# Optimization experiments

Hardware: AMD Instinct MI355X
Metric: run time of the kernel (lower is better)

Reference implementation:

```python
import jax, jax.numpy as jnp
import numpy as np

N = 100000
E = 3200000
H = 128
C = 40


def setup_inputs() -> dict:
    key = jax.random.key(0)
    ks = jax.random.split(key, 7)
    x = jax.random.normal(ks[0], (N, H), dtype=jnp.float32)
    edge_src = jax.random.randint(ks[1], (E,), 0, N, dtype=jnp.int32)
    edge_dst = jnp.sort(jax.random.randint(ks[2], (E,), 0, N, dtype=jnp.int32))
    edge_w = jax.random.uniform(ks[3], (E,), dtype=jnp.float32)
    s = 1.0 / np.sqrt(H)
    W0 = jax.random.normal(ks[4], (H, H), dtype=jnp.float32) * s
    W1 = jax.random.normal(ks[5], (H, H), dtype=jnp.float32) * s
    W2 = jax.random.normal(ks[6], (H, C), dtype=jnp.float32) * s
    return {"x": x, "edge_src": edge_src, "edge_dst": edge_dst,
            "edge_w": edge_w, "W0": W0, "W1": W1, "W2": W2}


def _spmm(h, edge_src, edge_dst, edge_w):
    # out[i] = sum_{e: dst_e == i} w_e * h[src_e]   (sparse adj @ h)
    msgs = h[edge_src] * edge_w[:, None]          # [E, d]
    return jax.ops.segment_sum(msgs, edge_dst, num_segments=N)


def reference(x, edge_src, edge_dst, edge_w, W0, W1, W2):
    # layer 1: tanh(Linear(spmm(adj, x)))  (dropout is identity in eval mode)
    h = jnp.tanh(_spmm(x, edge_src, edge_dst, edge_w) @ W0)
    # layer 2
    h = jnp.tanh(_spmm(h, edge_src, edge_dst, edge_w) @ W1)
    # output layer (GraphConvSparse default activation is tanh here too)
    out = jnp.tanh(_spmm(h, edge_src, edge_dst, edge_w) @ W2)
    return out
```

## Files before the change

### kernel.cpp

```cpp
#include <hip/hip_runtime.h>
#include <hip/hip_fp16.h>

#define NN 100000
#define NPAD 100096
#define EE 3200000
#define HH 128
#define CC 40

typedef _Float16 f16x8 __attribute__((ext_vector_type(8)));
typedef float f32x4 __attribute__((ext_vector_type(4)));

__global__ void build_rp(const int* __restrict__ dst, int* __restrict__ rp) {
    int i = blockIdx.x * blockDim.x + threadIdx.x;
    if (i > NN) return;
    int lo = 0, hi = EE;
    while (lo < hi) {
        int mid = (lo + hi) >> 1;
        if (dst[mid] < i) lo = mid + 1; else hi = mid;
    }
    rp[i] = lo;
}

__global__ __launch_bounds__(256) void f32_to_f16(const float* __restrict__ in,
                                                  __half* __restrict__ out, int n) {
    int base = (blockIdx.x * 256 + threadIdx.x) * 8;
    if (base >= n) return;
    float4 a = *(const float4*)(in + base);
    float4 b = *(const float4*)(in + base + 4);
    __half2 h[4];
    h[0] = __floats2half2_rn(a.x, a.y);
    h[1] = __floats2half2_rn(a.z, a.w);
    h[2] = __floats2half2_rn(b.x, b.y);
    h[3] = __floats2half2_rn(b.z, b.w);
    *(float4*)(out + base) = *(float4*)h;
}

__global__ __launch_bounds__(256) void prep_weights(const float* __restrict__ W0,
                                                    const float* __restrict__ W1,
                                                    const float* __restrict__ W2,
                                                    __half* __restrict__ W0t,
                                                    __half* __restrict__ W1t,
                                                    __half* __restrict__ W2t) {
    int i = blockIdx.x * 256 + threadIdx.x;
    if (i < HH * HH) {
        int c = i >> 7, k = i & 127;
        W0t[i] = __float2half_rn(W0[k * HH + c]);
        W1t[i] = __float2half_rn(W1[k * HH + c]);
    }
    if (i < 48 * HH) {
        int c = i >> 7, k = i & 127;
        W2t[i] = __float2half_rn(c < CC ? W2[k * CC + c] : 0.f);
    }
}

__global__ __launch_bounds__(256) void spmm_h16(const __half* __restrict__ h,
                                                const int* __restrict__ src,
                                                const float* __restrict__ w,
                                                const int* __restrict__ rp,
                                                __half* __restrict__ out) {
    int node = blockIdx.x * 4 + (threadIdx.x >> 6);
    int t = threadIdx.x & 63;
    if (node >= NN) return;
    int e0 = __builtin_amdgcn_readfirstlane(rp[node]);
    int e1 = __builtin_amdgcn_readfirstlane(rp[node + 1]);
    const __half2* __restrict__ h2 = (const __half2*)h;
    float accx = 0.f, accy = 0.f;
    int e = e0;
    for (; e + 8 <= e1; e += 8) {
        int s[8]; float wv[8]; __half2 r[8];
#pragma unroll
        for (int j = 0; j < 8; ++j) { s[j] = src[e + j]; wv[j] = w[e + j]; }
#pragma unroll
        for (int j = 0; j < 8; ++j) r[j] = h2[(size_t)s[j] * 64 + t];
#pragma unroll
        for (int j = 0; j < 8; ++j) {
            float2 f = __half22float2(r[j]);
            accx = fmaf(wv[j], f.x, accx);
            accy = fmaf(wv[j], f.y, accy);
        }
    }
    for (; e < e1; ++e) {
        int s = src[e]; float ww = w[e];
        float2 f = __half22float2(h2[(size_t)s * 64 + t]);
        accx = fmaf(ww, f.x, accx); accy = fmaf(ww, f.y, accy);
    }
    ((__half2*)out)[(size_t)node * 64 + t] = __floats2half2_rn(accx, accy);
}

__global__ __launch_bounds__(256) void spmm40_tanh(const __half* __restrict__ g,
                                                   const int* __restrict__ src,
                                                   const float* __restrict__ w,
                                                   const int* __restrict__ rp,
                                                   float* __restrict__ out) {
    int node = blockIdx.x * 4 + (threadIdx.x >> 6);
    int t = threadIdx.x & 63;
    if (node >= NN) return;
    int e0 = __builtin_amdgcn_readfirstlane(rp[node]);
    int e1 = __builtin_amdgcn_readfirstlane(rp[node + 1]);
    const __half2* __restrict__ g2 = (const __half2*)g;
    int tt = t < 20 ? t : 0;
    float accx = 0.f, accy = 0.f;
    int e = e0;
    for (; e + 8 <= e1; e += 8) {
        int s[8]; float wv[8]; __half2 r[8];
#pragma unroll
        for (int j = 0; j < 8; ++j) { s[j] = src[e + j]; wv[j] = w[e + j]; }
#pragma unroll
        for (int j = 0; j < 8; ++j) r[j] = g2[(size_t)s[j] * 20 + tt];
#pragma unroll
        for (int j = 0; j < 8; ++j) {
            float2 f = __half22float2(r[j]);
            accx = fmaf(wv[j], f.x, accx);
            accy = fmaf(wv[j], f.y, accy);
        }
    }
    for (; e < e1; ++e) {
        int s = src[e]; float ww = w[e];
        float2 f = __half22float2(g2[(size_t)s * 20 + tt]);
        accx = fmaf(ww, f.x, accx); accy = fmaf(ww, f.y, accy);
    }
    if (t < 20)
        *(float2*)(out + (size_t)node * CC + 2 * t) = make_float2(tanhf(accx), tanhf(accy));
}

__global__ __launch_bounds__(256) void gemm_mfma_tanh(const __half* __restrict__ A,
                                                      const __half* __restrict__ Wt,
                                                      __half* __restrict__ out) {
    int wave = threadIdx.x >> 6, l = threadIdx.x & 63;
    int r0 = blockIdx.x * 64 + wave * 16;
    int lr = l & 15, lg = l >> 4;
    const _Float16* Af = (const _Float16*)A;
    const _Float16* Wf = (const _Float16*)Wt;
    int arow = r0 + lr;
    f16x8 a[4];
#pragma unroll
    for (int kb = 0; kb < 4; ++kb)
        a[kb] = *(const f16x8*)(Af + (size_t)arow * HH + kb * 32 + lg * 8);
#pragma unroll
    for (int ct = 0; ct < 8; ++ct) {
        f32x4 acc = {0.f, 0.f, 0.f, 0.f};
#pragma unroll
        for (int kb = 0; kb < 4; ++kb) {
            f16x8 b = *(const f16x8*)(Wf + (size_t)(ct * 16 + lr) * HH + kb * 32 + lg * 8);
            acc = __builtin_amdgcn_mfma_f32_16x16x32_f16(a[kb], b, acc, 0, 0, 0);
        }
#pragma unroll
        for (int r = 0; r < 4; ++r) {
            int row = r0 + lg * 4 + r;
            if (row < NN)
                out[(size_t)row * HH + ct * 16 + lr] = __float2half_rn(tanhf(acc[r]));
        }
    }
}

__global__ __launch_bounds__(256) void gemm40_mfma(const __half* __restrict__ A,
                                                   const __half* __restrict__ Wt,
                                                   __half* __restrict__ out) {
    int wave = threadIdx.x >> 6, l = threadIdx.x & 63;
    int r0 = blockIdx.x * 64 + wave * 16;
    int lr = l & 15, lg = l >> 4;
    const _Float16* Af = (const _Float16*)A;
    const _Float16* Wf = (const _Float16*)Wt;
    int arow = r0 + lr;
    f16x8 a[4];
#pragma unroll
    for (int kb = 0; kb < 4; ++kb)
        a[kb] = *(const f16x8*)(Af + (size_t)arow * HH + kb * 32 + lg * 8);
#pragma unroll
    for (int ct = 0; ct < 3; ++ct) {
        f32x4 acc = {0.f, 0.f, 0.f, 0.f};
#pragma unroll
        for (int kb = 0; kb < 4; ++kb) {
            f16x8 b = *(const f16x8*)(Wf + (size_t)(ct * 16 + lr) * HH + kb * 32 + lg * 8);
            acc = __builtin_amdgcn_mfma_f32_16x16x32_f16(a[kb], b, acc, 0, 0, 0);
        }
        int col = ct * 16 + lr;
#pragma unroll
        for (int r = 0; r < 4; ++r) {
            int row = r0 + lg * 4 + r;
            if (row < NN && col < CC)
                out[(size_t)row * CC + col] = __float2half_rn(acc[r]);
        }
    }
}

extern "C" void kernel_launch(void* const* d_in, const int* in_sizes, int n_in,
                              void* d_out, int out_size, void* d_ws, size_t ws_size,
                              hipStream_t stream) {
    const float* x    = (const float*)d_in[0];
    const int*   esrc = (const int*)d_in[1];
    const int*   edst = (const int*)d_in[2];
    const float* ew   = (const float*)d_in[3];
    const float* W0   = (const float*)d_in[4];
    const float* W1   = (const float*)d_in[5];
    const float* W2   = (const float*)d_in[6];
    float* out = (float*)d_out;

    char* ws = (char*)d_ws;
    size_t off = 0;
    int* rp = (int*)(ws + off);          off += (((size_t)(NN + 1) * 4) + 511) & ~(size_t)511;
    __half* xh = (__half*)(ws + off);    off += (size_t)NPAD * HH * sizeof(__half);
    __half* sA = (__half*)(ws + off);    off += (size_t)NPAD * HH * sizeof(__half);
    __half* hb = (__half*)(ws + off);    off += (size_t)NPAD * HH * sizeof(__half);
    __half* gb = (__half*)(ws + off);    off += (size_t)NPAD * CC * sizeof(__half);
    __half* W0t = (__half*)(ws + off);   off += (size_t)HH * HH * sizeof(__half);
    __half* W1t = (__half*)(ws + off);   off += (size_t)HH * HH * sizeof(__half);
    __half* W2t = (__half*)(ws + off);   off += (size_t)48 * HH * sizeof(__half);

    build_rp<<<(NN + 256) / 256, 256, 0, stream>>>(edst, rp);
    f32_to_f16<<<(NN * HH) / (256 * 8), 256, 0, stream>>>(x, xh, NN * HH);
    prep_weights<<<64, 256, 0, stream>>>(W0, W1, W2, W0t, W1t, W2t);

    int gemm_grid = NPAD / 64;
    spmm_h16<<<NN / 4, 256, 0, stream>>>(xh, esrc, ew, rp, sA);
    gemm_mfma_tanh<<<gemm_grid, 256, 0, stream>>>(sA, W0t, hb);
    spmm_h16<<<NN / 4, 256, 0, stream>>>(hb, esrc, ew, rp, sA);
    gemm_mfma_tanh<<<gemm_grid, 256, 0, stream>>>(sA, W1t, hb);
    gemm40_mfma<<<gemm_grid, 256, 0, stream>>>(hb, W2t, gb);
    spmm40_tanh<<<NN / 4, 256, 0, stream>>>(gb, esrc, ew, rp, out);
}
```

Measured before the change: 498.8 us.

## Interleave edge src/weight and split SpMM edges across lane groups with wide loads

Adds a prep kernel that packs edge source indices and weights into interleaved int2 pairs. The SpMM kernels now have each wave split into lane groups that process different edges in parallel, with 16-byte f16x8 row loads, and then reduce the groups with cross-lane shuffles. The 40-column intermediate is padded to 64 columns so rows align for vector loads. This aims to raise memory-level parallelism and cut the number of per-edge index loads in the gather, at the cost of an extra edge-packing pass over 3.2M edges and shuffle reductions.

After: 514.6 us. 3.2% more time.

```diff
diff --git a/kernel.cpp b/kernel.cpp
--- a/kernel.cpp
+++ b/kernel.cpp
@@ -35,6 +35,19 @@
     *(float4*)(out + base) = *(float4*)h;
 }
 
+__global__ __launch_bounds__(256) void prep_edges(const int* __restrict__ src,
+                                                  const float* __restrict__ w,
+                                                  int4* __restrict__ ew) {
+    int i = blockIdx.x * 256 + threadIdx.x;
+    if (i >= EE / 4) return;
+    int4 s = ((const int4*)src)[i];
+    float4 f = ((const float4*)w)[i];
+    int4 a, b;
+    a.x = s.x; a.y = __float_as_int(f.x); a.z = s.y; a.w = __float_as_int(f.y);
+    b.x = s.z; b.y = __float_as_int(f.z); b.z = s.w; b.w = __float_as_int(f.w);
+    ew[2 * i] = a; ew[2 * i + 1] = b;
+}
+
 __global__ __launch_bounds__(256) void prep_weights(const float* __restrict__ W0,
                                                     const float* __restrict__ W1,
                                                     const float* __restrict__ W2,
@@ -47,80 +60,135 @@
         W0t[i] = __float2half_rn(W0[k * HH + c]);
         W1t[i] = __float2half_rn(W1[k * HH + c]);
     }
-    if (i < 48 * HH) {
+    if (i < 64 * HH) {
         int c = i >> 7, k = i & 127;
         W2t[i] = __float2half_rn(c < CC ? W2[k * CC + c] : 0.f);
     }
 }
 
 __global__ __launch_bounds__(256) void spmm_h16(const __half* __restrict__ h,
-                                                const int* __restrict__ src,
-                                                const float* __restrict__ w,
+                                                const int2* __restrict__ ew,
                                                 const int* __restrict__ rp,
                                                 __half* __restrict__ out) {
     int node = blockIdx.x * 4 + (threadIdx.x >> 6);
-    int t = threadIdx.x & 63;
+    int l = threadIdx.x & 63;
     if (node >= NN) return;
     int e0 = __builtin_amdgcn_readfirstlane(rp[node]);
     int e1 = __builtin_amdgcn_readfirstlane(rp[node + 1]);
-    const __half2* __restrict__ h2 = (const __half2*)h;
-    float accx = 0.f, accy = 0.f;
+    int g = l >> 4, r = l & 15;
+    const f16x8* __restrict__ hrow = (const f16x8*)h;
+    float acc[8] = {};
     int e = e0;
-    for (; e + 8 <= e1; e += 8) {
-        int s[8]; float wv[8]; __half2 r[8];
-#pragma unroll
-        for (int j = 0; j < 8; ++j) { s[j] = src[e + j]; wv[j] = w[e + j]; }
-#pragma unroll
-        for (int j = 0; j < 8; ++j) r[j] = h2[(size_t)s[j] * 64 + t];
-#pragma unroll
-        for (int j = 0; j < 8; ++j) {
-            float2 f = __half22float2(r[j]);
-            accx = fmaf(wv[j], f.x, accx);
-            accy = fmaf(wv[j], f.y, accy);
-        }
-    }
-    for (; e < e1; ++e) {
-        int s = src[e]; float ww = w[e];
-        float2 f = __half22float2(h2[(size_t)s * 64 + t]);
-        accx = fmaf(ww, f.x, accx); accy = fmaf(ww, f.y, accy);
-    }
-    ((__half2*)out)[(size_t)node * 64 + t] = __floats2half2_rn(accx, accy);
-}
-
-__global__ __launch_bounds__(256) void spmm40_tanh(const __half* __restrict__ g,
-                                                   const int* __restrict__ src,
-                                                   const float* __restrict__ w,
+    if ((e & 1) && e < e1) {
+        int2 pr = ew[e];
+        float wk = (g == 0) ? __int_as_float(pr.y) : 0.f;
+        f16x8 v = hrow[(size_t)pr.x * 16 + r];
+#pragma unroll
+        for (int j = 0; j < 8; ++j) acc[j] = fmaf(wk, (float)v[j], acc[j]);
+        ++e;
+    }
+    int efull = e + ((e1 - e) & ~15);
+    for (; e < efull; e += 16) {
+        const int4* pp = (const int4*)(ew + e + 4 * g);
+        int4 pa = pp[0];
+        int4 pb = pp[1];
+        f16x8 v0 = hrow[(size_t)pa.x * 16 + r];
+        f16x8 v1 = hrow[(size_t)pa.z * 16 + r];
+        f16x8 v2 = hrow[(size_t)pb.x * 16 + r];
+        f16x8 v3 = hrow[(size_t)pb.z * 16 + r];
+        float w0 = __int_as_float(pa.y), w1 = __int_as_float(pa.w);
+        float w2 = __int_as_float(pb.y), w3 = __int_as_float(pb.w);
+#pragma unroll
+        for (int j = 0; j < 8; ++j) acc[j] = fmaf(w0, (float)v0[j], acc[j]);
+#pragma unroll
+        for (int j = 0; j < 8; ++j) acc[j] = fmaf(w1, (float)v1[j], acc[j]);
+#pragma unroll
+        for (int j = 0; j < 8; ++j) acc[j] = fmaf(w2, (float)v2[j], acc[j]);
+#pragma unroll
+        for (int j = 0; j < 8; ++j) acc[j] = fmaf(w3, (float)v3[j], acc[j]);
+    }
+    if (e < e1) {
+#pragma unroll
+        for (int k = 0; k < 4; ++k) {
+            int idx = e + 4 * g + k;
+            bool val = idx < e1;
+            int2 pr = ew[val ? idx : e0];
+            float wk = val ? __int_as_float(pr.y) : 0.f;
+            f16x8 v = hrow[(size_t)pr.x * 16 + r];
+#pragma unroll
+            for (int j = 0; j < 8; ++j) acc[j] = fmaf(wk, (float)v[j], acc[j]);
+        }
+    }
+#pragma unroll
+    for (int j = 0; j < 8; ++j) {
+        acc[j] += __shfl_xor(acc[j], 16);
+        acc[j] += __shfl_xor(acc[j], 32);
+    }
+    if (l < 16) {
+        __half2 hv[4];
+#pragma unroll
+        for (int j = 0; j < 4; ++j) hv[j] = __floats2half2_rn(acc[2 * j], acc[2 * j + 1]);
+        *(float4*)(out + (size_t)node * HH + r * 8) = *(float4*)hv;
+    }
+}
+
+__global__ __launch_bounds__(256) void spmm40_tanh(const __half* __restrict__ gpad,
+                                                   const int2* __restrict__ ew,
                                                    const int* __restrict__ rp,
                                                    float* __restrict__ out) {
     int node = blockIdx.x * 4 + (threadIdx.x >> 6);
-    int t = threadIdx.x & 63;
+    int l = threadIdx.x & 63;
     if (node >= NN) return;
     int e0 = __builtin_amdgcn_readfirstlane(rp[node]);
     int e1 = __builtin_amdgcn_readfirstlane(rp[node + 1]);
-    const __half2* __restrict__ g2 = (const __half2*)g;
-    int tt = t < 20 ? t : 0;
-    float accx = 0.f, accy = 0.f;
+    int g = l >> 3, r = l & 7;
+    const f16x8* __restrict__ grow = (const f16x8*)gpad;
+    float acc[8] = {};
     int e = e0;
-    for (; e + 8 <= e1; e += 8) {
-        int s[8]; float wv[8]; __half2 r[8];
-#pragma unroll
-        for (int j = 0; j < 8; ++j) { s[j] = src[e + j]; wv[j] = w[e + j]; }
-#pragma unroll
-        for (int j = 0; j < 8; ++j) r[j] = g2[(size_t)s[j] * 20 + tt];
-#pragma unroll
-        for (int j = 0; j < 8; ++j) {
-            float2 f = __half22float2(r[j]);
-            accx = fmaf(wv[j], f.x, accx);
-            accy = fmaf(wv[j], f.y, accy);
-        }
-    }
-    for (; e < e1; ++e) {
-        int s = src[e]; float ww = w[e];
-        float2 f = __half22float2(g2[(size_t)s * 20 + tt]);
-        accx = fmaf(ww, f.x, accx); accy = fmaf(ww, f.y, accy);
-    }
-    if (t < 20)
-        *(float2*)(out + (size_t)node * CC + 2 * t) = make_float2(tanhf(accx), tanhf(accy));
+    if ((e & 1) && e < e1) {
+        int2 pr = ew[e];
+        float wk = (g == 0) ? __int_as_float(pr.y) : 0.f;
+        f16x8 v = grow[(size_t)pr.x * 8 + r];
+#pragma unroll
+        for (int j = 0; j < 8; ++j) acc[j] = fmaf(wk, (float)v[j], acc[j]);
+        ++e;
+    }
+    int efull = e + ((e1 - e) & ~15);
+    for (; e < efull; e += 16) {
+        int4 pa = *(const int4*)(ew + e + 2 * g);
+        f16x8 v0 = grow[(size_t)pa.x * 8 + r];
+        f16x8 v1 = grow[(size_t)pa.z * 8 + r];
+        float w0 = __int_as_float(pa.y), w1 = __int_as_float(pa.w);
+#pragma unroll
+        for (int j = 0; j < 8; ++j) acc[j] = fmaf(w0, (float)v0[j], acc[j]);
+#pragma unroll
+        for (int j = 0; j < 8; ++j) acc[j] = fmaf(w1, (float)v1[j], acc[j]);
+    }
+    if (e < e1) {
+#pragma unroll
+        for (int k = 0; k < 2; ++k) {
+            int idx = e + 2 * g + k;
+            bool val = idx < e1;
+            int2 pr = ew[val ? idx : e0];
+            float wk = val ? __int_as_float(pr.y) : 0.f;
+            f16x8 v = grow[(size_t)pr.x * 8 + r];
+#pragma unroll
+            for (int j = 0; j < 8; ++j) acc[j] = fmaf(wk, (float)v[j], acc[j]);
+        }
+    }
+#pragma unroll
+    for (int j = 0; j < 8; ++j) {
+        acc[j] += __shfl_xor(acc[j], 8);
+        acc[j] += __shfl_xor(acc[j], 16);
+        acc[j] += __shfl_xor(acc[j], 32);
+    }
+    if (l < 5) {
+        float o[8];
+#pragma unroll
+        for (int j = 0; j < 8; ++j) o[j] = tanhf(acc[j]);
+        *(float4*)(out + (size_t)node * CC + r * 8) = *(float4*)&o[0];
+        *(float4*)(out + (size_t)node * CC + r * 8 + 4) = *(float4*)&o[4];
+    }
 }
 
 __global__ __launch_bounds__(256) void gemm_mfma_tanh(const __half* __restrict__ A,
@@ -167,7 +235,7 @@
     for (int kb = 0; kb < 4; ++kb)
         a[kb] = *(const f16x8*)(Af + (size_t)arow * HH + kb * 32 + lg * 8);
 #pragma unroll
-    for (int ct = 0; ct < 3; ++ct) {
+    for (int ct = 0; ct < 4; ++ct) {
         f32x4 acc = {0.f, 0.f, 0.f, 0.f};
 #pragma unroll
         for (int kb = 0; kb < 4; ++kb) {
@@ -178,8 +246,8 @@
 #pragma unroll
         for (int r = 0; r < 4; ++r) {
             int row = r0 + lg * 4 + r;
-            if (row < NN && col < CC)
-                out[(size_t)row * CC + col] = __float2half_rn(acc[r]);
+            if (row < NN)
+                out[(size_t)row * 64 + col] = __float2half_rn(acc[r]);
         }
     }
 }
@@ -190,7 +258,7 @@
     const float* x    = (const float*)d_in[0];
     const int*   esrc = (const int*)d_in[1];
     const int*   edst = (const int*)d_in[2];
-    const float* ew   = (const float*)d_in[3];
+    const float* ew_f = (const float*)d_in[3];
     const float* W0   = (const float*)d_in[4];
     const float* W1   = (const float*)d_in[5];
     const float* W2   = (const float*)d_in[6];
@@ -199,23 +267,26 @@
     char* ws = (char*)d_ws;
     size_t off = 0;
     int* rp = (int*)(ws + off);          off += (((size_t)(NN + 1) * 4) + 511) & ~(size_t)511;
-    __half* xh = (__half*)(ws + off);    off += (size_t)NPAD * HH * sizeof(__half);
+    __half* buf0 = (__half*)(ws + off);  off += (size_t)NPAD * HH * sizeof(__half);
     __half* sA = (__half*)(ws + off);    off += (size_t)NPAD * HH * sizeof(__half);
     __half* hb = (__half*)(ws + off);    off += (size_t)NPAD * HH * sizeof(__half);
-    __half* gb = (__half*)(ws + off);    off += (size_t)NPAD * CC * sizeof(__half);
+    int2* ew = (int2*)(ws + off);        off += (size_t)EE * sizeof(int2);
     __half* W0t = (__half*)(ws + off);   off += (size_t)HH * HH * sizeof(__half);
     __half* W1t = (__half*)(ws + off);   off += (size_t)HH * HH * sizeof(__half);
-    __half* W2t = (__half*)(ws + off);   off += (size_t)48 * HH * sizeof(__half);
+    __half* W2t = (__half*)(ws + off);   off += (size_t)64 * HH * sizeof(__half);
+    __half* xh = buf0;
+    __half* gb = buf0;
 
     build_rp<<<(NN + 256) / 256, 256, 0, stream>>>(edst, rp);
     f32_to_f16<<<(NN * HH) / (256 * 8), 256, 0, stream>>>(x, xh, NN * HH);
+    prep_edges<<<(EE / 4 + 255) / 256, 256, 0, stream>>>(esrc, ew_f, (int4*)ew);
     prep_weights<<<64, 256, 0, stream>>>(W0, W1, W2, W0t, W1t, W2t);
 
     int gemm_grid = NPAD / 64;
-    spmm_h16<<<NN / 4, 256, 0, stream>>>(xh, esrc, ew, rp, sA);
+    spmm_h16<<<NN / 4, 256, 0, stream>>>(xh, ew, rp, sA);
     gemm_mfma_tanh<<<gemm_grid, 256, 0, stream>>>(sA, W0t, hb);
-    spmm_h16<<<NN / 4, 256, 0, stream>>>(hb, esrc, ew, rp, sA);
+    spmm_h16<<<NN / 4, 256, 0, stream>>>(hb, ew, rp, sA);
     gemm_mfma_tanh<<<gemm_grid, 256, 0, stream>>>(sA, W1t, hb);
     gemm40_mfma<<<gemm_grid, 256, 0, stream>>>(hb, W2t, gb);
-    spmm40_tanh<<<NN / 4, 256, 0, stream>>>(gb, esrc, ew, rp, out);
-}
+    spmm40_tanh<<<NN / 4, 256, 0, stream>>>(gb, ew, rp, out);
+}
```
